# Performance work log

Hardware: AMD Instinct MI355X
Metric: run time of the kernel (lower is better)

The kernel has to match this reference:

```python
import jax, jax.numpy as jnp
import numpy as np

# Faithful JAX port of Attention_concat (concat-style PAM).
# The original intent: energy[b,i,j] = concat_conv([q[b,:,i]; k[b,:,j]]) which is
# algebraically separable: energy = (q^T wq)[:, :, None] + (k^T wk)[:, None, :].
# attention = energy / (H*W) (no softmax), out = value @ attention, out = gamma*out + x.

B, C, H, W = 4, 256, 64, 64
K_RED = 4
INTER = C // K_RED  # 64


def setup_inputs() -> dict:
    key = jax.random.key(0)
    ks = jax.random.split(key, 9)
    s = 0.02
    x = jax.random.normal(ks[0], (B, C, H, W), dtype=jnp.float32)
    Wq = jax.random.normal(ks[1], (INTER, C), dtype=jnp.float32) * s
    bq = jax.random.normal(ks[2], (INTER,), dtype=jnp.float32) * s
    Wk = jax.random.normal(ks[3], (INTER, C), dtype=jnp.float32) * s
    bk = jax.random.normal(ks[4], (INTER,), dtype=jnp.float32) * s
    Wc = jax.random.normal(ks[5], (2 * INTER,), dtype=jnp.float32) * s  # concat_conv weight, no bias
    Wv = jax.random.normal(ks[6], (C, C), dtype=jnp.float32) * s
    bv = jax.random.normal(ks[7], (C,), dtype=jnp.float32) * s
    gamma = jax.random.normal(ks[8], (1,), dtype=jnp.float32) * 0.1  # nonzero so output depends on attention
    return {"x": x, "Wq": Wq, "bq": bq, "Wk": Wk, "bk": bk, "Wc": Wc, "Wv": Wv, "bv": bv, "gamma": gamma}


def reference(x, Wq, bq, Wk, bk, Wc, Wv, bv, gamma):
    b, c, h, w = x.shape
    n = h * w
    inter = Wq.shape[0]
    xf = x.reshape(b, c, n)  # [B, C, N]
    # 1x1 convs == per-position channel matmuls
    q = jnp.einsum("bcn,oc->bon", xf, Wq) + bq[None, :, None]  # [B, inter, N]
    k = jnp.einsum("bcn,oc->bon", xf, Wk) + bk[None, :, None]  # [B, inter, N]
    wq, wk = Wc[:inter], Wc[inter:]
    # separable concat-conv score: energy[b,i,j] = <q[b,:,i], wq> + <k[b,:,j], wk>
    eq = jnp.einsum("bcn,c->bn", q, wq)  # [B, N]
    ek = jnp.einsum("bcn,c->bn", k, wk)  # [B, N]
    attention = (eq[:, :, None] + ek[:, None, :]) / jnp.asarray(n, x.dtype)  # [B, N, N]
    v = jnp.einsum("bcn,oc->bon", xf, Wv) + bv[None, :, None]  # [B, C, N]
    out = jnp.einsum("bcn,bnm->bcm", v, attention).reshape(b, c, h, w)
    return gamma * out + x
```

## Files before the change

kernel.cpp:

```cpp
#include <hip/hip_runtime.h>

#define B_DIM 4
#define C_DIM 256
#define N_DIM 4096
#define INTER 64
#define LDS_PAD 68

#define EK_OFF   0
#define PSEQ_OFF 16384
#define PSX_OFF  16640
#define PSXE_OFF 82176
#define SV_OFF   147712
#define SVE_OFF  148736

__device__ inline float wave_red_sum(float v) {
    #pragma unroll
    for (int off = 32; off > 0; off >>= 1) v += __shfl_down(v, off, 64);
    return v;
}

__global__ __launch_bounds__(256) void k_fuse(
        const float* __restrict__ x,
        const float* __restrict__ Wq, const float* __restrict__ bq,
        const float* __restrict__ Wk, const float* __restrict__ bk,
        const float* __restrict__ Wc, float* __restrict__ ws) {
    __shared__ float xt[C_DIM][LDS_PAD];
    __shared__ float uqs[C_DIM], uks[C_DIM];
    __shared__ float sq[4][64], sk[4][64];
    __shared__ float eq_s[64];
    __shared__ float cqk[2];
    const int t  = threadIdx.x;
    const int nb = blockIdx.x;
    const int b  = blockIdx.y;
    const int n0 = nb * 64;

    {
        float uq = 0.f, uk = 0.f;
        #pragma unroll 8
        for (int o = 0; o < INTER; ++o) {
            uq = fmaf(Wc[o],         Wq[o * C_DIM + t], uq);
            uk = fmaf(Wc[INTER + o], Wk[o * C_DIM + t], uk);
        }
        uqs[t] = uq; uks[t] = uk;
        if (t == 0) { float s = 0.f; for (int o = 0; o < INTER; ++o) s = fmaf(Wc[o], bq[o], s); cqk[0] = s; }
        if (t == 1) { float s = 0.f; for (int o = 0; o < INTER; ++o) s = fmaf(Wc[INTER + o], bk[o], s); cqk[1] = s; }
    }

    const float4* x4 = (const float4*)x;
    #pragma unroll
    for (int i = 0; i < 16; ++i) {
        const int f = i * 256 + t;
        const int c = f >> 4, q = f & 15;
        float4 v = x4[((size_t)b * C_DIM + c) * (N_DIM / 4) + (n0 >> 2) + q];
        *(float4*)&xt[c][4 * q] = v;
    }
    __syncthreads();

    const int w = t >> 6, l = t & 63;
    {
        float aq = 0.f, ak = 0.f;
        const int cb = w * 64;
        #pragma unroll 16
        for (int c = 0; c < 64; ++c) {
            float xv = xt[cb + c][l];
            aq = fmaf(uqs[cb + c], xv, aq);
            ak = fmaf(uks[cb + c], xv, ak);
        }
        sq[w][l] = aq; sk[w][l] = ak;
    }
    __syncthreads();
    if (w == 0) {
        float tq = sq[0][l] + sq[1][l] + sq[2][l] + sq[3][l] + cqk[0];
        float tk = sk[0][l] + sk[1][l] + sk[2][l] + sk[3][l] + cqk[1];
        ws[EK_OFF + b * N_DIM + n0 + l] = tk;
        eq_s[l] = tq;
        float se = wave_red_sum(tq);
        if (l == 0) ws[PSEQ_OFF + b * 64 + nb] = se;
    }
    __syncthreads();

    {
        float sx = 0.f, sxe = 0.f;
        const float4* row = (const float4*)&xt[t][0];
        const float4* ev  = (const float4*)&eq_s[0];
        #pragma unroll
        for (int i = 0; i < 16; ++i) {
            float4 xv = row[i];
            float4 e  = ev[i];
            sx += xv.x + xv.y + xv.z + xv.w;
            sxe = fmaf(xv.x, e.x, sxe); sxe = fmaf(xv.y, e.y, sxe);
            sxe = fmaf(xv.z, e.z, sxe); sxe = fmaf(xv.w, e.w, sxe);
        }
        ws[PSX_OFF  + (size_t)(b * 64 + nb) * C_DIM + t] = sx;
        ws[PSXE_OFF + (size_t)(b * 64 + nb) * C_DIM + t] = sxe;
    }
}

__global__ __launch_bounds__(256) void k_sv2(
        const float* __restrict__ Wv, const float* __restrict__ bv,
        const float* __restrict__ ws_ro, float* __restrict__ ws) {
    const int cg = blockIdx.x;
    const int b  = blockIdx.y;
    const int t  = threadIdx.x;
    __shared__ float sSx[C_DIM], sSxe[C_DIM];
    __shared__ float sSeq;
    float sx = 0.f, sxe = 0.f;
    #pragma unroll 8
    for (int nb = 0; nb < 64; ++nb) {
        sx  += ws_ro[PSX_OFF  + (size_t)(b * 64 + nb) * C_DIM + t];
        sxe += ws_ro[PSXE_OFF + (size_t)(b * 64 + nb) * C_DIM + t];
    }
    sSx[t] = sx; sSxe[t] = sxe;
    if (t < 64) {
        float se = wave_red_sum(ws_ro[PSEQ_OFF + b * 64 + t]);
        if (t == 0) sSeq = se;
    }
    __syncthreads();
    const int cl = t >> 2, s = t & 3;
    const int c  = cg * 64 + cl;
    const float4* wr = (const float4*)(Wv + (size_t)c * C_DIM + 64 * s);
    float sv = 0.f, sve = 0.f;
    #pragma unroll
    for (int i = 0; i < 16; ++i) {
        float4 wv4 = wr[i];
        const int base = 64 * s + 4 * i;
        sv  = fmaf(wv4.x, sSx[base],     sv);
        sv  = fmaf(wv4.y, sSx[base + 1], sv);
        sv  = fmaf(wv4.z, sSx[base + 2], sv);
        sv  = fmaf(wv4.w, sSx[base + 3], sv);
        sve = fmaf(wv4.x, sSxe[base],     sve);
        sve = fmaf(wv4.y, sSxe[base + 1], sve);
        sve = fmaf(wv4.z, sSxe[base + 2], sve);
        sve = fmaf(wv4.w, sSxe[base + 3], sve);
    }
    sv  += __shfl_down(sv, 2, 64);  sv  += __shfl_down(sv, 1, 64);
    sve += __shfl_down(sve, 2, 64); sve += __shfl_down(sve, 1, 64);
    if (s == 0) {
        ws[SV_OFF  + b * C_DIM + c] = sv + (float)N_DIM * bv[c];
        ws[SVE_OFF + b * C_DIM + c] = sve + bv[c] * sSeq;
    }
}

__global__ __launch_bounds__(256) void k_out(
        const float* __restrict__ x, const float* __restrict__ ws,
        const float* __restrict__ gamma, float* __restrict__ out) {
    const float ginv = gamma[0] / (float)N_DIM;
    const size_t total4 = (size_t)B_DIM * C_DIM * N_DIM / 4;
    for (size_t i = (size_t)blockIdx.x * blockDim.x + threadIdx.x; i < total4;
         i += (size_t)gridDim.x * blockDim.x) {
        const size_t e = i * 4;
        const int m  = (int)(e & (N_DIM - 1));
        const int bc = (int)(e >> 12);
        const int b  = bc >> 8;
        const float4 xv  = ((const float4*)x)[i];
        const float4 ekv = *(const float4*)(ws + EK_OFF + (size_t)b * N_DIM + m);
        const float t1 = ws[SV_OFF  + bc] * ginv;
        const float t2 = ws[SVE_OFF + bc] * ginv;
        float4 o;
        o.x = fmaf(ekv.x, t1, t2) + xv.x;
        o.y = fmaf(ekv.y, t1, t2) + xv.y;
        o.z = fmaf(ekv.z, t1, t2) + xv.z;
        o.w = fmaf(ekv.w, t1, t2) + xv.w;
        ((float4*)out)[i] = o;
    }
}

extern "C" void kernel_launch(void* const* d_in, const int* in_sizes, int n_in,
                              void* d_out, int out_size, void* d_ws, size_t ws_size,
                              hipStream_t stream) {
    const float* x     = (const float*)d_in[0];
    const float* Wq    = (const float*)d_in[1];
    const float* bq    = (const float*)d_in[2];
    const float* Wk    = (const float*)d_in[3];
    const float* bk    = (const float*)d_in[4];
    const float* Wc    = (const float*)d_in[5];
    const float* Wv    = (const float*)d_in[6];
    const float* bv    = (const float*)d_in[7];
    const float* gamma = (const float*)d_in[8];
    float* out = (float*)d_out;
    float* ws  = (float*)d_ws;

    dim3 gA(N_DIM / 64, B_DIM);
    k_fuse<<<gA, 256, 0, stream>>>(x, Wq, bq, Wk, bk, Wc, ws);

    dim3 gB(4, B_DIM);
    k_sv2<<<gB, 256, 0, stream>>>(Wv, bv, ws, ws);

    k_out<<<4096, 256, 0, stream>>>(x, ws, gamma, out);
}
```

Measured before the change: 104.8 us.

## Fuse three kernels into one cooperative kernel with grid sync, reuse LDS x tile

Merges the reduction, Wv matvec and output kernels into a single cooperative launch of 256 blocks separated by a grid-wide barrier. The x tile stays in LDS so the output pass does not re-read x from global memory, and two kernel launches plus the ek workspace round trip go away. In exchange every block redundantly reduces the partial sums and computes the full 256x256 Wv matvec for its batch. It also adds grid-sync overhead and needs all 256 blocks to be co-resident.

```diff
diff --git a/kernel.cpp b/kernel.cpp
--- a/kernel.cpp
+++ b/kernel.cpp
@@ -1,4 +1,6 @@
 #include <hip/hip_runtime.h>
+#include <hip/hip_cooperative_groups.h>
+namespace cg = cooperative_groups;
 
 #define B_DIM 4
 #define C_DIM 256
@@ -6,12 +8,9 @@
 #define INTER 64
 #define LDS_PAD 68
 
-#define EK_OFF   0
-#define PSEQ_OFF 16384
-#define PSX_OFF  16640
-#define PSXE_OFF 82176
-#define SV_OFF   147712
-#define SVE_OFF  148736
+#define PSEQ_OFF 0
+#define PSX_OFF  256
+#define PSXE_OFF (256 + 65536)
 
 __device__ inline float wave_red_sum(float v) {
     #pragma unroll
@@ -19,20 +18,26 @@
     return v;
 }
 
-__global__ __launch_bounds__(256) void k_fuse(
+__global__ __launch_bounds__(256) void k_all(
         const float* __restrict__ x,
         const float* __restrict__ Wq, const float* __restrict__ bq,
         const float* __restrict__ Wk, const float* __restrict__ bk,
-        const float* __restrict__ Wc, float* __restrict__ ws) {
+        const float* __restrict__ Wc, const float* __restrict__ Wv,
+        const float* __restrict__ bv, const float* __restrict__ gamma,
+        float* __restrict__ ws, float* __restrict__ out)
+{
     __shared__ float xt[C_DIM][LDS_PAD];
     __shared__ float uqs[C_DIM], uks[C_DIM];
     __shared__ float sq[4][64], sk[4][64];
-    __shared__ float eq_s[64];
+    __shared__ float eq_s[64], ek_s[64];
     __shared__ float cqk[2];
+    __shared__ float sSeq;
+
     const int t  = threadIdx.x;
-    const int nb = blockIdx.x;
-    const int b  = blockIdx.y;
+    const int nb = blockIdx.x & 63;
+    const int b  = blockIdx.x >> 6;
     const int n0 = nb * 64;
+    const int w  = t >> 6, l = t & 63;
 
     {
         float uq = 0.f, uk = 0.f;
@@ -56,7 +61,6 @@
     }
     __syncthreads();
 
-    const int w = t >> 6, l = t & 63;
     {
         float aq = 0.f, ak = 0.f;
         const int cb = w * 64;
@@ -72,8 +76,7 @@
     if (w == 0) {
         float tq = sq[0][l] + sq[1][l] + sq[2][l] + sq[3][l] + cqk[0];
         float tk = sk[0][l] + sk[1][l] + sk[2][l] + sk[3][l] + cqk[1];
-        ws[EK_OFF + b * N_DIM + n0 + l] = tk;
-        eq_s[l] = tq;
+        eq_s[l] = tq; ek_s[l] = tk;
         float se = wave_red_sum(tq);
         if (l == 0) ws[PSEQ_OFF + b * 64 + nb] = se;
     }
@@ -94,74 +97,64 @@
         ws[PSX_OFF  + (size_t)(b * 64 + nb) * C_DIM + t] = sx;
         ws[PSXE_OFF + (size_t)(b * 64 + nb) * C_DIM + t] = sxe;
     }
-}
 
-__global__ __launch_bounds__(256) void k_sv2(
-        const float* __restrict__ Wv, const float* __restrict__ bv,
-        const float* __restrict__ ws_ro, float* __restrict__ ws) {
-    const int cg = blockIdx.x;
-    const int b  = blockIdx.y;
-    const int t  = threadIdx.x;
-    __shared__ float sSx[C_DIM], sSxe[C_DIM];
-    __shared__ float sSeq;
-    float sx = 0.f, sxe = 0.f;
-    #pragma unroll 8
-    for (int nb = 0; nb < 64; ++nb) {
-        sx  += ws_ro[PSX_OFF  + (size_t)(b * 64 + nb) * C_DIM + t];
-        sxe += ws_ro[PSXE_OFF + (size_t)(b * 64 + nb) * C_DIM + t];
-    }
-    sSx[t] = sx; sSxe[t] = sxe;
-    if (t < 64) {
-        float se = wave_red_sum(ws_ro[PSEQ_OFF + b * 64 + t]);
-        if (t == 0) sSeq = se;
+    cg::this_grid().sync();
+
+    {
+        float sx = 0.f, sxe = 0.f;
+        #pragma unroll 8
+        for (int j = 0; j < 64; ++j) {
+            sx  += ws[PSX_OFF  + (size_t)(b * 64 + j) * C_DIM + t];
+            sxe += ws[PSXE_OFF + (size_t)(b * 64 + j) * C_DIM + t];
+        }
+        ((float*)sq)[t] = sx;
+        ((float*)sk)[t] = sxe;
+        if (w == 0) {
+            float se = wave_red_sum(ws[PSEQ_OFF + b * 64 + l]);
+            if (l == 0) sSeq = se;
+        }
     }
     __syncthreads();
-    const int cl = t >> 2, s = t & 3;
-    const int c  = cg * 64 + cl;
-    const float4* wr = (const float4*)(Wv + (size_t)c * C_DIM + 64 * s);
-    float sv = 0.f, sve = 0.f;
-    #pragma unroll
-    for (int i = 0; i < 16; ++i) {
-        float4 wv4 = wr[i];
-        const int base = 64 * s + 4 * i;
-        sv  = fmaf(wv4.x, sSx[base],     sv);
-        sv  = fmaf(wv4.y, sSx[base + 1], sv);
-        sv  = fmaf(wv4.z, sSx[base + 2], sv);
-        sv  = fmaf(wv4.w, sSx[base + 3], sv);
-        sve = fmaf(wv4.x, sSxe[base],     sve);
-        sve = fmaf(wv4.y, sSxe[base + 1], sve);
-        sve = fmaf(wv4.z, sSxe[base + 2], sve);
-        sve = fmaf(wv4.w, sSxe[base + 3], sve);
+    {
+        const float* sSx  = (const float*)sq;
+        const float* sSxe = (const float*)sk;
+        const float4* wr = (const float4*)(Wv + (size_t)t * C_DIM);
+        float sv = 0.f, sve = 0.f;
+        #pragma unroll 8
+        for (int i = 0; i < 64; ++i) {
+            float4 w4 = wr[i];
+            const int e = 4 * i;
+            sv  = fmaf(w4.x, sSx[e],     sv);
+            sv  = fmaf(w4.y, sSx[e + 1], sv);
+            sv  = fmaf(w4.z, sSx[e + 2], sv);
+            sv  = fmaf(w4.w, sSx[e + 3], sv);
+            sve = fmaf(w4.x, sSxe[e],     sve);
+            sve = fmaf(w4.y, sSxe[e + 1], sve);
+            sve = fmaf(w4.z, sSxe[e + 2], sve);
+            sve = fmaf(w4.w, sSxe[e + 3], sve);
+        }
+        const float ginv = gamma[0] / (float)N_DIM;
+        uqs[t] = (sv  + (float)N_DIM * bv[t]) * ginv;
+        uks[t] = (sve + bv[t] * sSeq) * ginv;
     }
-    sv  += __shfl_down(sv, 2, 64);  sv  += __shfl_down(sv, 1, 64);
-    sve += __shfl_down(sve, 2, 64); sve += __shfl_down(sve, 1, 64);
-    if (s == 0) {
-        ws[SV_OFF  + b * C_DIM + c] = sv + (float)N_DIM * bv[c];
-        ws[SVE_OFF + b * C_DIM + c] = sve + bv[c] * sSeq;
-    }
-}
+    __syncthreads();
 
-__global__ __launch_bounds__(256) void k_out(
-        const float* __restrict__ x, const float* __restrict__ ws,
-        const float* __restrict__ gamma, float* __restrict__ out) {
-    const float ginv = gamma[0] / (float)N_DIM;
-    const size_t total4 = (size_t)B_DIM * C_DIM * N_DIM / 4;
-    for (size_t i = (size_t)blockIdx.x * blockDim.x + threadIdx.x; i < total4;
-         i += (size_t)gridDim.x * blockDim.x) {
-        const size_t e = i * 4;
-        const int m  = (int)(e & (N_DIM - 1));
-        const int bc = (int)(e >> 12);
-        const int b  = bc >> 8;
-        const float4 xv  = ((const float4*)x)[i];
-        const float4 ekv = *(const float4*)(ws + EK_OFF + (size_t)b * N_DIM + m);
-        const float t1 = ws[SV_OFF  + bc] * ginv;
-        const float t2 = ws[SVE_OFF + bc] * ginv;
-        float4 o;
-        o.x = fmaf(ekv.x, t1, t2) + xv.x;
-        o.y = fmaf(ekv.y, t1, t2) + xv.y;
-        o.z = fmaf(ekv.z, t1, t2) + xv.z;
-        o.w = fmaf(ekv.w, t1, t2) + xv.w;
-        ((float4*)out)[i] = o;
+    {
+        float4* o4 = (float4*)out;
+        const int q = t & 15;
+        const float4 ek4 = *(const float4*)&ek_s[4 * q];
+        #pragma unroll
+        for (int i = 0; i < 16; ++i) {
+            const int c = i * 16 + (t >> 4);
+            const float4 xv = *(const float4*)&xt[c][4 * q];
+            const float t1 = uqs[c], t2 = uks[c];
+            float4 o;
+            o.x = fmaf(ek4.x, t1, t2) + xv.x;
+            o.y = fmaf(ek4.y, t1, t2) + xv.y;
+            o.z = fmaf(ek4.z, t1, t2) + xv.z;
+            o.w = fmaf(ek4.w, t1, t2) + xv.w;
+            o4[((size_t)b * C_DIM + c) * (N_DIM / 4) + (n0 >> 2) + q] = o;
+        }
     }
 }
 
@@ -180,11 +173,9 @@
     float* out = (float*)d_out;
     float* ws  = (float*)d_ws;
 
-    dim3 gA(N_DIM / 64, B_DIM);
-    k_fuse<<<gA, 256, 0, stream>>>(x, Wq, bq, Wk, bk, Wc, ws);
-
-    dim3 gB(4, B_DIM);
-    k_sv2<<<gB, 256, 0, stream>>>(Wv, bv, ws, ws);
-
-    k_out<<<4096, 256, 0, stream>>>(x, ws, gamma, out);
+    void* args[] = { (void*)&x, (void*)&Wq, (void*)&bq, (void*)&Wk, (void*)&bk,
+                     (void*)&Wc, (void*)&Wv, (void*)&bv, (void*)&gamma,
+                     (void*)&ws, (void*)&out };
+    hipLaunchCooperativeKernel((const void*)k_all, dim3(B_DIM * 64), dim3(256),
+                               args, 0, stream);
 }
```

After: 144.1 us. 37.4% more time.
